# Kernel optimization log

Hardware: AMD Instinct MI355X
Metric: run time of the kernel (lower is better)

The kernel has to match this reference:

```python
import jax, jax.numpy as jnp
import numpy as np

N_NODES = 50000
N_EDGES = 250000
N_GRAPHS = 512
F_IN = 32
F_EDGE = 16
LATENT = 32
EMBED = 128


def setup_inputs() -> dict:
    key = jax.random.key(0)
    ks = jax.random.split(key, 10)
    x = jax.random.normal(ks[0], (N_NODES, F_IN), dtype=jnp.float32)
    edge_index = jax.random.randint(ks[1], (2, N_EDGES), 0, N_NODES, dtype=jnp.int64)
    edge_attr = jax.random.normal(ks[2], (N_EDGES, F_EDGE), dtype=jnp.float32)
    batch = jnp.sort(jax.random.randint(ks[3], (N_NODES,), 0, N_GRAPHS, dtype=jnp.int64))
    s = 0.05
    W1 = jax.random.normal(ks[4], (F_EDGE, LATENT), dtype=jnp.float32) * s
    b1 = jnp.zeros((LATENT,), jnp.float32)
    W2 = jax.random.normal(ks[5], (LATENT, F_IN * LATENT), dtype=jnp.float32) * s
    b2 = jnp.zeros((F_IN * LATENT,), jnp.float32)
    root = jax.random.normal(ks[6], (F_IN, LATENT), dtype=jnp.float32) * s
    conv_bias = jnp.zeros((LATENT,), jnp.float32)
    fc_w = jax.random.normal(ks[7], (LATENT, EMBED), dtype=jnp.float32) * s
    fc_b = jnp.zeros((EMBED,), jnp.float32)
    return dict(x=x, edge_index=edge_index, edge_attr=edge_attr, batch=batch,
                W1=W1, b1=b1, W2=W2, b2=b2, root=root, conv_bias=conv_bias,
                fc_w=fc_w, fc_b=fc_b)


def reference(x, edge_index, edge_attr, batch, W1, b1, W2, b2, root, conv_bias, fc_w, fc_b):
    src, dst = edge_index[0], edge_index[1]
    # edge MLP: [E, F_edge] -> [E, F_in*latent] -> [E, F_in, latent]
    h = jax.nn.relu(edge_attr @ W1 + b1)
    ew = (h @ W2 + b2).reshape(-1, F_IN, LATENT)
    # per-edge matvec: message_e = x[src_e] @ W_e
    msg = jnp.einsum('ef,efl->el', x[src], ew)
    # scatter-add to target nodes (NNConv default aggr='add')
    agg = jax.ops.segment_sum(msg, dst, num_segments=N_NODES)
    node = jax.nn.relu(agg + x @ root + conv_bias)
    # global mean pool per graph
    sums = jax.ops.segment_sum(node, batch, num_segments=N_GRAPHS)
    cnts = jax.ops.segment_sum(jnp.ones((node.shape[0],), node.dtype), batch, num_segments=N_GRAPHS)
    pooled = sums / jnp.maximum(cnts, 1.0)[:, None]
    return jax.nn.relu(pooled) @ fc_w + fc_b
```

## Files before the change

kernel.cpp:

```cpp
#include <hip/hip_runtime.h>
#include <hip/hip_fp16.h>

#define N_NODES 50000
#define N_EDGES 250000
#define N_GRAPHS 512
#define F_IN 32
#define F_EDGE 16
#define LATENT 32
#define EMBED 128
#define E_BLK 256
#define N_EBLK ((N_EDGES + E_BLK - 1) / E_BLK)
#define KW 1056
#define HS_STRIDE 36

typedef unsigned short ushort;
typedef unsigned int uint;
typedef _Float16 half8v __attribute__((ext_vector_type(8)));
typedef _Float16 half2v __attribute__((ext_vector_type(2)));
typedef __attribute__((ext_vector_type(4))) float f32x4;

union UH8 { half8v h8; half2v h2[4]; ushort u[8]; uint q[4]; };
union UH2 { half2v h2; uint q; };

__device__ inline ushort f2h_bits(float f) {
    _Float16 h = (_Float16)f;
    return *reinterpret_cast<ushort*>(&h);
}

__global__ void prep_kernel(const float* __restrict__ W2, const float* __restrict__ b2,
                            ushort* __restrict__ W2T, uint4* __restrict__ aggz,
                            float* __restrict__ pool, float* __restrict__ pcnt) {
    int i = blockIdx.x * blockDim.x + threadIdx.x;
    if (i < (N_NODES * LATENT * 2) / 16) aggz[i] = make_uint4(0u, 0u, 0u, 0u);
    if (i < 32 * 1024) {
        int kk = i >> 5, l = i & 31;
        W2T[l * KW + kk] = f2h_bits(W2[i]);
    }
    if (i < 1024) {
        int f = i >> 5, l = i & 31;
        W2T[l * KW + 1024 + f] = f2h_bits(b2[i]);
    }
    if (i < N_GRAPHS * LATENT) pool[i] = 0.f;
    if (i < N_GRAPHS) pcnt[i] = 0.f;
}

__global__ __launch_bounds__(512) void edge_mfma_kernel(
    const float* __restrict__ x, const int* __restrict__ ei,
    const float* __restrict__ ea, const float* __restrict__ W1,
    const float* __restrict__ b1, const ushort* __restrict__ W2T,
    __half* __restrict__ aggh)
{
    __shared__ __attribute__((aligned(16))) ushort Hs[E_BLK * HS_STRIDE];
    __shared__ __attribute__((aligned(16))) ushort W2q[32 * 256];

    const int t = threadIdx.x;
    const int e0 = blockIdx.x * E_BLK;
    const int wv = t >> 6, lane = t & 63;
    const int g = lane >> 4, j16 = lane & 15;

    UH8 bw[2];
    #pragma unroll
    for (int nt = 0; nt < 2; ++nt) {
        #pragma unroll
        for (int b = 0; b < 8; ++b) {
            float w = (g < 2) ? W1[(8 * g + b) * LATENT + nt * 16 + j16] : 0.f;
            bw[nt].u[b] = f2h_bits(w);
        }
    }
    float b1v[2] = { b1[j16], b1[16 + j16] };

    #pragma unroll
    for (int mt = 0; mt < 2; ++mt) {
        int mtg = 2 * wv + mt;
        int rowA = mtg * 16 + j16;
        int e = e0 + rowA; if (e >= N_EDGES) e = N_EDGES - 1;
        UH8 ae;
        if (g < 2) {
            const float4* p = (const float4*)(ea + (size_t)e * F_EDGE + 8 * g);
            float4 va = p[0], vb = p[1];
            ae.u[0] = f2h_bits(va.x); ae.u[1] = f2h_bits(va.y);
            ae.u[2] = f2h_bits(va.z); ae.u[3] = f2h_bits(va.w);
            ae.u[4] = f2h_bits(vb.x); ae.u[5] = f2h_bits(vb.y);
            ae.u[6] = f2h_bits(vb.z); ae.u[7] = f2h_bits(vb.w);
        } else {
            ae.q[0] = 0; ae.q[1] = 0; ae.q[2] = 0; ae.q[3] = 0;
        }
        #pragma unroll
        for (int nt = 0; nt < 2; ++nt) {
            f32x4 hacc = (f32x4){0.f, 0.f, 0.f, 0.f};
            hacc = __builtin_amdgcn_mfma_f32_16x16x32_f16(ae.h8, bw[nt].h8, hacc, 0, 0, 0);
            #pragma unroll
            for (int v = 0; v < 4; ++v) {
                int rowD = mtg * 16 + 4 * g + v;
                int col = nt * 16 + j16;
                float hval = fmaxf(hacc[v] + b1v[nt], 0.f);
                Hs[rowD * HS_STRIDE + col] = f2h_bits(hval);
            }
        }
    }

    f32x4 acc[2][2];
    #pragma unroll
    for (int a = 0; a < 2; ++a)
        #pragma unroll
        for (int b = 0; b < 2; ++b) acc[a][b] = (f32x4){0.f, 0.f, 0.f, 0.f};

    UH8 xf[2];
    int myrow[2];
    #pragma unroll
    for (int mt = 0; mt < 2; ++mt) {
        int row = (2 * wv + mt) * 16 + j16;
        myrow[mt] = row;
        int e = e0 + row; if (e >= N_EDGES) e = N_EDGES - 1;
        int src = ei[e];
        const float4* p = (const float4*)(x + (size_t)src * F_IN + 8 * g);
        float4 va = p[0], vb = p[1];
        xf[mt].u[0] = f2h_bits(va.x); xf[mt].u[1] = f2h_bits(va.y);
        xf[mt].u[2] = f2h_bits(va.z); xf[mt].u[3] = f2h_bits(va.w);
        xf[mt].u[4] = f2h_bits(vb.x); xf[mt].u[5] = f2h_bits(vb.y);
        xf[mt].u[6] = f2h_bits(vb.z); xf[mt].u[7] = f2h_bits(vb.w);
    }

    {
        UH8 bx0, bx1;
        *(uint4*)bx0.q = *(const uint4*)(W2T + (size_t)j16 * KW + 1024 + 8 * g);
        *(uint4*)bx1.q = *(const uint4*)(W2T + (size_t)(16 + j16) * KW + 1024 + 8 * g);
        #pragma unroll
        for (int mt = 0; mt < 2; ++mt) {
            acc[mt][0] = __builtin_amdgcn_mfma_f32_16x16x32_f16(xf[mt].h8, bx0.h8, acc[mt][0], 0, 0, 0);
            acc[mt][1] = __builtin_amdgcn_mfma_f32_16x16x32_f16(xf[mt].h8, bx1.h8, acc[mt][1], 0, 0, 0);
        }
    }

    for (int q = 0; q < 4; ++q) {
        if (q) __syncthreads();
        #pragma unroll
        for (int c = 0; c < 2; ++c) {
            int ch = c * 512 + t;
            int lbyte = ch * 16;
            int jrow = lbyte >> 9;
            int off = lbyte & 511;
            uint4 val = *(const uint4*)((const char*)W2T + (size_t)jrow * (KW * 2) + q * 512 + off);
            *(uint4*)((char*)W2q + jrow * 512 + (off ^ ((jrow & 7) << 4))) = val;
        }
        __syncthreads();

        uint hbp[2][8];
        #pragma unroll
        for (int mt = 0; mt < 2; ++mt) {
            const ushort* hp = Hs + myrow[mt] * HS_STRIDE + q * 8;
            uint2 ra = *(const uint2*)hp;
            uint2 rb = *(const uint2*)(hp + 4);
            uint raw[4] = { ra.x, ra.y, rb.x, rb.y };
            #pragma unroll
            for (int i = 0; i < 4; ++i) {
                uint u = raw[i];
                hbp[mt][2 * i]     = (u & 0xFFFFu) * 0x10001u;
                hbp[mt][2 * i + 1] = (u >> 16) * 0x10001u;
            }
        }

        #pragma unroll
        for (int kst = 0; kst < 8; ++kst) {
            int kb = kst * 64 + g * 16;
            UH8 bf0, bf1;
            *(uint4*)bf0.q = *(const uint4*)((const char*)W2q + j16 * 512 + (kb ^ ((j16 & 7) << 4)));
            *(uint4*)bf1.q = *(const uint4*)((const char*)W2q + (16 + j16) * 512 + (kb ^ ((j16 & 7) << 4)));
            #pragma unroll
            for (int mt = 0; mt < 2; ++mt) {
                UH2 h2; h2.q = hbp[mt][kst];
                UH8 af;
                #pragma unroll
                for (int p = 0; p < 4; ++p) af.h2[p] = h2.h2 * xf[mt].h2[p];
                acc[mt][0] = __builtin_amdgcn_mfma_f32_16x16x32_f16(af.h8, bf0.h8, acc[mt][0], 0, 0, 0);
                acc[mt][1] = __builtin_amdgcn_mfma_f32_16x16x32_f16(af.h8, bf1.h8, acc[mt][1], 0, 0, 0);
            }
        }
    }

    const int odd = j16 & 1;
    #pragma unroll
    for (int mt = 0; mt < 2; ++mt) {
        int rowb = (2 * wv + mt) * 16 + 4 * g;
        #pragma unroll
        for (int v = 0; v < 4; ++v) {
            int e = e0 + rowb + v;
            float a0 = acc[mt][0][v], a1 = acc[mt][1][v];
            float p0 = __shfl_xor(a0, 1);
            float p1 = __shfl_xor(a1, 1);
            if (e < N_EDGES) {
                int dst = ei[N_EDGES + e];
                __half2 hv = odd ? __floats2half2_rn(p1, a1) : __floats2half2_rn(a0, p0);
                int col = odd ? (15 + j16) : j16;
                unsafeAtomicAdd((__half2*)(aggh + (size_t)dst * LATENT + col), hv);
            }
        }
    }
}

#define VN 8
__global__ __launch_bounds__(256) void nodepool_kernel(
    const float* __restrict__ x, const __half* __restrict__ aggh,
    const float* __restrict__ root, const float* __restrict__ cbias,
    const int* __restrict__ batch, float* __restrict__ pool,
    float* __restrict__ pcnt)
{
    int t = threadIdx.x;
    int l = t & 31;
    int stripe = t >> 5;
    int v0 = (blockIdx.x * 8 + stripe) * VN;
    float rc[F_IN];
    #pragma unroll
    for (int f = 0; f < F_IN; ++f) rc[f] = root[f * LATENT + l];
    float cbl = cbias[l];

    float sum = 0.f, cnt = 0.f;
    int gcur = -1;
    for (int i = 0; i < VN; ++i) {
        int v = v0 + i;
        if (v >= N_NODES) break;
        int g = batch[v];
        if (g != gcur) {
            if (gcur >= 0) {
                atomicAdd(&pool[gcur * LATENT + l], sum);
                if (l == 0) atomicAdd(&pcnt[gcur], cnt);
            }
            gcur = g; sum = 0.f; cnt = 0.f;
        }
        float xv = x[(size_t)v * F_IN + l];
        float a = __half2float(aggh[(size_t)v * LATENT + l]) + cbl;
        #pragma unroll
        for (int f = 0; f < F_IN; ++f) {
            float xfv = __shfl(xv, (t & 32) | f);
            a += xfv * rc[f];
        }
        sum += fmaxf(a, 0.f);
        cnt += 1.f;
    }
    if (gcur >= 0) {
        atomicAdd(&pool[gcur * LATENT + l], sum);
        if (l == 0) atomicAdd(&pcnt[gcur], cnt);
    }
}

__global__ void final_kernel(const float* __restrict__ pool, const float* __restrict__ pcnt,
                             const float* __restrict__ fcw, const float* __restrict__ fcb,
                             float* __restrict__ out)
{
    int t = blockIdx.x * blockDim.x + threadIdx.x;
    int gr = t >> 7, j = t & 127;
    if (gr >= N_GRAPHS) return;
    float inv = 1.0f / fmaxf(pcnt[gr], 1.0f);
    float o = fcb[j];
    #pragma unroll 8
    for (int l = 0; l < LATENT; ++l) {
        float pv = fmaxf(pool[gr * LATENT + l] * inv, 0.0f);
        o += pv * fcw[l * EMBED + j];
    }
    out[gr * EMBED + j] = o;
}

extern "C" void kernel_launch(void* const* d_in, const int* in_sizes, int n_in,
                              void* d_out, int out_size, void* d_ws, size_t ws_size,
                              hipStream_t stream)
{
    const float* x     = (const float*)d_in[0];
    const int*   ei    = (const int*)d_in[1];
    const float* ea    = (const float*)d_in[2];
    const int*   batch = (const int*)d_in[3];
    const float* W1    = (const float*)d_in[4];
    const float* b1    = (const float*)d_in[5];
    const float* W2    = (const float*)d_in[6];
    const float* b2    = (const float*)d_in[7];
    const float* root  = (const float*)d_in[8];
    const float* cb    = (const float*)d_in[9];
    const float* fcw   = (const float*)d_in[10];
    const float* fcb   = (const float*)d_in[11];
    float* out = (float*)d_out;

    char* w = (char*)d_ws;
    auto alloc = [&](size_t bytes) {
        char* p = w;
        w += (bytes + 255) & ~size_t(255);
        return p;
    };
    ushort* W2T  = (ushort*)alloc((size_t)32 * KW * 2);
    __half* aggh = (__half*)alloc((size_t)N_NODES * LATENT * 2);
    float*  pool = (float*)alloc(N_GRAPHS * LATENT * 4);
    float*  pcnt = (float*)alloc(N_GRAPHS * 4);

    prep_kernel<<<782, 256, 0, stream>>>(W2, b2, W2T, (uint4*)aggh, pool, pcnt);
    edge_mfma_kernel<<<N_EBLK, 512, 0, stream>>>(x, ei, ea, W1, b1, W2T, aggh);
    nodepool_kernel<<<(N_NODES + 8 * VN - 1) / (8 * VN), 256, 0, stream>>>(
        x, aggh, root, cb, batch, pool, pcnt);
    final_kernel<<<(N_GRAPHS * EMBED + 255) / 256, 256, 0, stream>>>(pool, pcnt, fcw, fcb, out);
}
```

Before: 62.78 us.

## Replace fp16 atomic scatter-add with CSR build and per-node gather

Builds a destination-sorted CSR on the device with three new kernels: a degree histogram, a single-block scan and a scatter of edge ids. The edge kernel now writes each fp16 message to a per-edge buffer instead of doing half2 atomic adds into node rows. The node kernel then sums each node's incoming messages by walking the CSR before applying root, ReLU and pooling. This removes atomic contention on the node aggregate. In exchange it adds three launches, a serial one-block scan, and a 16 MB message buffer that is written and then read back through indirect gathers.

```diff
diff --git a/kernel.cpp b/kernel.cpp
--- a/kernel.cpp
+++ b/kernel.cpp
@@ -28,10 +28,10 @@
 }
 
 __global__ void prep_kernel(const float* __restrict__ W2, const float* __restrict__ b2,
-                            ushort* __restrict__ W2T, uint4* __restrict__ aggz,
+                            ushort* __restrict__ W2T, int* __restrict__ deg,
                             float* __restrict__ pool, float* __restrict__ pcnt) {
     int i = blockIdx.x * blockDim.x + threadIdx.x;
-    if (i < (N_NODES * LATENT * 2) / 16) aggz[i] = make_uint4(0u, 0u, 0u, 0u);
+    if (i < N_NODES) deg[i] = 0;
     if (i < 32 * 1024) {
         int kk = i >> 5, l = i & 31;
         W2T[l * KW + kk] = f2h_bits(W2[i]);
@@ -42,13 +42,70 @@
     }
     if (i < N_GRAPHS * LATENT) pool[i] = 0.f;
     if (i < N_GRAPHS) pcnt[i] = 0.f;
+}
+
+__global__ void hist_kernel(const int* __restrict__ ei, int* __restrict__ deg) {
+    int e = blockIdx.x * blockDim.x + threadIdx.x;
+    if (e < N_EDGES) atomicAdd(&deg[ei[N_EDGES + e]], 1);
+}
+
+__global__ __launch_bounds__(1024) void scan_kernel(const int* __restrict__ deg,
+                                                    int* __restrict__ off,
+                                                    int* __restrict__ cursor) {
+    __shared__ int wsum[16];
+    const int CH = 49;
+    int t = threadIdx.x;
+    int s = t * CH;
+    int sum = 0;
+    for (int i = 0; i < CH; ++i) {
+        int idx = s + i;
+        sum += (idx < N_NODES) ? deg[idx] : 0;
+    }
+    int lane = t & 63, wid = t >> 6;
+    int inc = sum;
+    #pragma unroll
+    for (int d = 1; d < 64; d <<= 1) {
+        int o = __shfl_up(inc, d);
+        if (lane >= d) inc += o;
+    }
+    if (lane == 63) wsum[wid] = inc;
+    __syncthreads();
+    if (t < 16) {
+        int wv = wsum[t];
+        int winc = wv;
+        #pragma unroll
+        for (int d = 1; d < 16; d <<= 1) {
+            int o = __shfl_up(winc, d);
+            if (t >= d) winc += o;
+        }
+        wsum[t] = winc - wv;
+    }
+    __syncthreads();
+    int run = wsum[wid] + (inc - sum);
+    for (int i = 0; i < CH; ++i) {
+        int idx = s + i;
+        if (idx < N_NODES) {
+            int d = deg[idx];
+            off[idx] = run; cursor[idx] = run; run += d;
+        }
+    }
+    if (t == 1023) off[N_NODES] = run;
+}
+
+__global__ void scatter_kernel(const int* __restrict__ ei, int* __restrict__ cursor,
+                               int* __restrict__ csr) {
+    int e = blockIdx.x * blockDim.x + threadIdx.x;
+    if (e < N_EDGES) {
+        int p = atomicAdd(&cursor[ei[N_EDGES + e]], 1);
+        csr[p] = e;
+    }
 }
 
 __global__ __launch_bounds__(512) void edge_mfma_kernel(
     const float* __restrict__ x, const int* __restrict__ ei,
     const float* __restrict__ ea, const float* __restrict__ W1,
     const float* __restrict__ b1, const ushort* __restrict__ W2T,
-    __half* __restrict__ aggh)
+    __half* __restrict__ msg)
 {
     __shared__ __attribute__((aligned(16))) ushort Hs[E_BLK * HS_STRIDE];
     __shared__ __attribute__((aligned(16))) ushort W2q[32 * 256];
@@ -189,18 +246,18 @@
             float p0 = __shfl_xor(a0, 1);
             float p1 = __shfl_xor(a1, 1);
             if (e < N_EDGES) {
-                int dst = ei[N_EDGES + e];
                 __half2 hv = odd ? __floats2half2_rn(p1, a1) : __floats2half2_rn(a0, p0);
                 int col = odd ? (15 + j16) : j16;
-                unsafeAtomicAdd((__half2*)(aggh + (size_t)dst * LATENT + col), hv);
+                *(__half2*)(msg + (size_t)e * LATENT + col) = hv;
             }
         }
     }
 }
 
 #define VN 8
-__global__ __launch_bounds__(256) void nodepool_kernel(
-    const float* __restrict__ x, const __half* __restrict__ aggh,
+__global__ __launch_bounds__(256) void gather_pool_kernel(
+    const float* __restrict__ x, const __half* __restrict__ msg,
+    const int* __restrict__ off, const int* __restrict__ csr,
     const float* __restrict__ root, const float* __restrict__ cbias,
     const int* __restrict__ batch, float* __restrict__ pool,
     float* __restrict__ pcnt)
@@ -228,7 +285,12 @@
             gcur = g; sum = 0.f; cnt = 0.f;
         }
         float xv = x[(size_t)v * F_IN + l];
-        float a = __half2float(aggh[(size_t)v * LATENT + l]) + cbl;
+        float a = cbl;
+        int p0 = off[v], p1 = off[v + 1];
+        for (int p = p0; p < p1; ++p) {
+            int e = csr[p];
+            a += __half2float(msg[(size_t)e * LATENT + l]);
+        }
         #pragma unroll
         for (int f = 0; f < F_IN; ++f) {
             float xfv = __shfl(xv, (t & 32) | f);
@@ -284,14 +346,21 @@
         w += (bytes + 255) & ~size_t(255);
         return p;
     };
-    ushort* W2T  = (ushort*)alloc((size_t)32 * KW * 2);
-    __half* aggh = (__half*)alloc((size_t)N_NODES * LATENT * 2);
-    float*  pool = (float*)alloc(N_GRAPHS * LATENT * 4);
-    float*  pcnt = (float*)alloc(N_GRAPHS * 4);
-
-    prep_kernel<<<782, 256, 0, stream>>>(W2, b2, W2T, (uint4*)aggh, pool, pcnt);
-    edge_mfma_kernel<<<N_EBLK, 512, 0, stream>>>(x, ei, ea, W1, b1, W2T, aggh);
-    nodepool_kernel<<<(N_NODES + 8 * VN - 1) / (8 * VN), 256, 0, stream>>>(
-        x, aggh, root, cb, batch, pool, pcnt);
+    ushort* W2T    = (ushort*)alloc((size_t)32 * KW * 2);
+    __half* msg    = (__half*)alloc((size_t)N_EDGES * LATENT * 2);
+    int*    deg    = (int*)alloc(N_NODES * 4);
+    int*    off    = (int*)alloc((N_NODES + 1) * 4);
+    int*    cursor = (int*)alloc(N_NODES * 4);
+    int*    csr    = (int*)alloc(N_EDGES * 4);
+    float*  pool   = (float*)alloc(N_GRAPHS * LATENT * 4);
+    float*  pcnt   = (float*)alloc(N_GRAPHS * 4);
+
+    prep_kernel<<<196, 256, 0, stream>>>(W2, b2, W2T, deg, pool, pcnt);
+    hist_kernel<<<(N_EDGES + 255) / 256, 256, 0, stream>>>(ei, deg);
+    scan_kernel<<<1, 1024, 0, stream>>>(deg, off, cursor);
+    scatter_kernel<<<(N_EDGES + 255) / 256, 256, 0, stream>>>(ei, cursor, csr);
+    edge_mfma_kernel<<<N_EBLK, 512, 0, stream>>>(x, ei, ea, W1, b1, W2T, msg);
+    gather_pool_kernel<<<(N_NODES + 8 * VN - 1) / (8 * VN), 256, 0, stream>>>(
+        x, msg, off, csr, root, cb, batch, pool, pcnt);
     final_kernel<<<(N_GRAPHS * EMBED + 255) / 256, 256, 0, stream>>>(pool, pcnt, fcw, fcb, out);
 }
```

After: 228.1 us. +263.3%, slower.
